# Optimization experiments

Hardware: AMD Instinct MI355X
Metric: run time of the kernel (lower is better)

Reference implementation:

```python
import jax, jax.numpy as jnp
import numpy as np

B, W, K = 16, 128, 128          # batch, window_size, n_features
KS = 7                          # conv kernel size
HG = 256                        # gru_hid_dim
HF = 256                        # forecast_hid_dim
HR = 256                        # recon_hid_dim
OUT = 128                       # out_dim
ALPHA = 0.2                     # leaky relu slope
ED = 2 * W                      # gatv2 embed dims (2*window == 2*features here == 256)


def setup_inputs() -> dict:
    key = jax.random.key(0)
    ks = jax.random.split(key, 32)
    s = lambda k, shp, sc=0.05: (jax.random.normal(k, shp, dtype=jnp.float32) * sc)
    return {
        "x": jax.random.normal(ks[0], (B, W, K), dtype=jnp.float32),
        # ConvLayer
        "conv_w": s(ks[1], (K, K, KS)),
        "conv_b": s(ks[2], (K,)),
        # FeatureAttentionLayer (gatv2): lin 2W->2W, a (2W,1), bias (K,K)
        "fg_lin_w": s(ks[3], (ED, 2 * W)),
        "fg_lin_b": s(ks[4], (ED,)),
        "fg_a": s(ks[5], (ED, 1)),
        "fg_bias": s(ks[6], (K, K)),
        # TemporalAttentionLayer (gatv2): lin 2K->2K, a (2K,1), bias (W,W)
        "tg_lin_w": s(ks[7], (2 * K, 2 * K)),
        "tg_lin_b": s(ks[8], (2 * K,)),
        "tg_a": s(ks[9], (2 * K, 1)),
        "tg_bias": s(ks[10], (W, W)),
        # GRU encoder: input 3K -> HG (torch gate order r,z,n)
        "gru_w_ih": s(ks[11], (3 * HG, 3 * K)),
        "gru_w_hh": s(ks[12], (3 * HG, HG)),
        "gru_b_ih": s(ks[13], (3 * HG,)),
        "gru_b_hh": s(ks[14], (3 * HG,)),
        # Forecasting_Model (n_layers=1 -> two Linears)
        "fc1_w": s(ks[15], (HF, HG)),
        "fc1_b": s(ks[16], (HF,)),
        "fc2_w": s(ks[17], (OUT, HF)),
        "fc2_b": s(ks[18], (OUT,)),
        # ReconstructionModel: decoder GRU HG -> HR, fc HR -> OUT
        "dec_w_ih": s(ks[19], (3 * HR, HG)),
        "dec_w_hh": s(ks[20], (3 * HR, HR)),
        "dec_b_ih": s(ks[21], (3 * HR,)),
        "dec_b_hh": s(ks[22], (3 * HR,)),
        "rec_fc_w": s(ks[23], (OUT, HR)),
        "rec_fc_b": s(ks[24], (OUT,)),
    }


def _gru(x_seq, w_ih, w_hh, b_ih, b_hh):
    """torch-convention GRU over (b, t, d). Returns (outs (b,t,H), h_T (b,H))."""
    H = w_hh.shape[1]
    def step(h, xt):
        gi = xt @ w_ih.T + b_ih
        gh = h @ w_hh.T + b_hh
        ir, iz, inn = jnp.split(gi, 3, axis=-1)
        hr, hz, hn = jnp.split(gh, 3, axis=-1)
        r = jax.nn.sigmoid(ir + hr)
        z = jax.nn.sigmoid(iz + hz)
        n = jnp.tanh(inn + r * hn)
        h_new = (1.0 - z) * n + z * h
        return h_new, h_new
    h0 = jnp.zeros((x_seq.shape[0], H), x_seq.dtype)
    hT, outs = jax.lax.scan(step, h0, jnp.swapaxes(x_seq, 0, 1))
    return jnp.swapaxes(outs, 0, 1), hT


def _gatv2(v, lin_w, lin_b, a, bias):
    """v: (b, N, D). Pairwise concat GATv2 attention, returns sigmoid(attn @ v)."""
    b, N, D = v.shape
    vi = jnp.broadcast_to(v[:, :, None, :], (b, N, N, D))   # node i repeated
    vj = jnp.broadcast_to(v[:, None, :, :], (b, N, N, D))   # node j alternating
    cat = jnp.concatenate([vi, vj], axis=-1)                 # (b, N, N, 2D)
    h = jax.nn.leaky_relu(cat @ lin_w.T + lin_b, ALPHA)      # (b, N, N, ED)
    e = jnp.squeeze(h @ a, -1) + bias                        # (b, N, N)
    attn = jax.nn.softmax(e, axis=2)
    return jax.nn.sigmoid(jnp.einsum('bij,bjd->bid', attn, v))


def reference(x, conv_w, conv_b, fg_lin_w, fg_lin_b, fg_a, fg_bias,
              tg_lin_w, tg_lin_b, tg_a, tg_bias,
              gru_w_ih, gru_w_hh, gru_b_ih, gru_b_hh,
              fc1_w, fc1_b, fc2_w, fc2_b,
              dec_w_ih, dec_w_hh, dec_b_ih, dec_b_hh, rec_fc_w, rec_fc_b):
    # ConvLayer: permute -> pad -> conv1d -> relu -> permute
    xc = jnp.transpose(x, (0, 2, 1))                        # (b, K, W)
    xc = jnp.pad(xc, ((0, 0), (0, 0), ((KS - 1) // 2, (KS - 1) // 2)))
    y = jax.lax.conv_general_dilated(xc, conv_w, (1,), 'VALID',
                                     dimension_numbers=('NCH', 'OIH', 'NCH'))
    xconv = jnp.transpose(jax.nn.relu(y + conv_b[None, :, None]), (0, 2, 1))  # (b, W, K)

    # Feature GAT operates on (b, K, W); output permuted back to (b, W, K)
    h_feat = jnp.transpose(
        _gatv2(jnp.transpose(xconv, (0, 2, 1)), fg_lin_w, fg_lin_b, fg_a, fg_bias),
        (0, 2, 1))
    # Temporal GAT operates on (b, W, K)
    h_temp = _gatv2(xconv, tg_lin_w, tg_lin_b, tg_a, tg_bias)

    h_cat = jnp.concatenate([xconv, h_feat, h_temp], axis=2)  # (b, W, 3K)
    _, h_end = _gru(h_cat, gru_w_ih, gru_w_hh, gru_b_ih, gru_b_hh)  # (b, HG)

    # Forecasting MLP (dropout is identity in eval)
    pred = jax.nn.relu(h_end @ fc1_w.T + fc1_b) @ fc2_w.T + fc2_b   # (b, OUT)

    # ReconstructionModel: repeat_interleave along dim=1 then view (b, W, HG)
    h_rep = jnp.repeat(h_end, W, axis=1).reshape(h_end.shape[0], W, -1)
    dec_out, _ = _gru(h_rep, dec_w_ih, dec_w_hh, dec_b_ih, dec_b_hh)  # (b, W, HR)
    recons = dec_out @ rec_fc_w.T + rec_fc_b                          # (b, W, OUT)

    return pred, recons
```

## Files before the change

### kernel.cpp

```cpp
#include <hip/hip_runtime.h>

typedef _Float16 f16;
typedef _Float16 f16x2 __attribute__((ext_vector_type(2)));
typedef _Float16 f16x4 __attribute__((ext_vector_type(4)));
typedef _Float16 f16x8 __attribute__((ext_vector_type(8)));
typedef float f32x4 __attribute__((ext_vector_type(4)));
typedef unsigned int ui4 __attribute__((ext_vector_type(4)));

__device__ __forceinline__ float fast_rcp(float x) {
#if __has_builtin(__builtin_amdgcn_rcpf)
    return __builtin_amdgcn_rcpf(x);
#else
    return 1.0f / x;
#endif
}
__device__ __forceinline__ float sigmoidf(float x) { return fast_rcp(1.0f + __expf(-x)); }
__device__ __forceinline__ float tanh_f(float x)   { return 2.0f * fast_rcp(1.0f + __expf(-2.0f * x)) - 1.0f; }

__device__ __forceinline__ unsigned int pk2(float a, float b) {
    union { _Float16 h[2]; unsigned int u; } t;
    t.h[0] = (_Float16)a; t.h[1] = (_Float16)b;
    return t.u;
}
__device__ __forceinline__ unsigned short f16bits(float f) {
    union { _Float16 h; unsigned short u; } t; t.h = (_Float16)f; return t.u;
}
__device__ __forceinline__ float dot2f(unsigned int wa, unsigned int hb, float c) {
#if __has_builtin(__builtin_amdgcn_fdot2)
    return __builtin_amdgcn_fdot2(__builtin_bit_cast(f16x2, wa),
                                  __builtin_bit_cast(f16x2, hb), c, false);
#else
    f16x2 a = __builtin_bit_cast(f16x2, wa), b = __builtin_bit_cast(f16x2, hb);
    return c + (float)a.x * (float)b.x + (float)a.y * (float)b.y;
#endif
}


__global__ void prep_kernel(const float* __restrict__ conv_w,
                            const float* __restrict__ fg_lin_w,
                            const float* __restrict__ tg_lin_w,
                            const float* __restrict__ w_ih,
                            const float* __restrict__ w_hh,
                            const float* __restrict__ dec_w_ih,
                            const float* __restrict__ dec_w_hh,
                            const float* __restrict__ rec_fc_w,
                            f16* __restrict__ w_ihB,
                            unsigned int* __restrict__ wpkE,
                            unsigned int* __restrict__ wpkD,
                            float* __restrict__ c01,
                            float* __restrict__ linTf, float* __restrict__ linTt,
                            float* __restrict__ recT, float* __restrict__ convT)
{
    const int blk = blockIdx.x, lane = threadIdx.x;
    const int quad = lane >> 4, lq = lane & 15;
    if (blk < 576) {
        int tau = blk / 12, kk = blk % 12;
        int g = tau % 3, jt = tau / 3;
        int n = g * 256 + jt * 16 + lq;
        int k0 = kk * 32 + quad * 8;
        f16x8 v;
#pragma unroll
        for (int e = 0; e < 8; ++e) v[e] = (f16)w_ih[n * 384 + k0 + e];
        *(f16x8*)&w_ihB[(blk * 64 + lane) * 8] = v;
    } else if (blk < 960) {
        int i2 = blk - 576;
        const float* src = w_hh; unsigned int* dst = wpkE;
        if (i2 >= 192) { i2 -= 192; src = dec_w_hh; dst = wpkD; }
        int g = i2 >> 6, i = i2 & 63;
#pragma unroll
        for (int c = 0; c < 8; ++c) {
            int tidx = lane * 8 + c;
            int j = tidx >> 1, half = tidx & 1;
            int n = g * 256 + j, k = half * 128 + i * 2;
            dst[(g * 64 + i) * 512 + tidx] = pk2(src[n * 256 + k], src[n * 256 + k + 1]);
        }
    } else if (blk < 972) {
        int n = (blk - 960) * 64 + lane;
        float s0 = 0.f, s1 = 0.f;
        const float* row = dec_w_ih + (long)n * 256;
        for (int d = 0; d < 128; ++d) { s0 += row[d]; s1 += row[128 + d]; }
        c01[n] = s0; c01[768 + n] = s1;
    } else if (blk < 1484) {
        int i = blk - 972; int mat = i >> 8, d = i & 255;
        const float* src = mat ? tg_lin_w : fg_lin_w;
        float* dst = mat ? linTt : linTf;
#pragma unroll
        for (int c = 0; c < 4; ++c) { int n = lane + 64 * c; dst[d * 256 + n] = src[n * 256 + d]; }
    } else if (blk < 1740) {
        int d = blk - 1484;
#pragma unroll
        for (int c = 0; c < 2; ++c) { int j2 = lane + 64 * c; recT[d * 128 + j2] = rec_fc_w[j2 * 256 + d]; }
    } else {
        int i = blk - 1740;
#pragma unroll
        for (int c = 0; c < 2; ++c) { int co = lane + 64 * c; convT[i * 128 + co] = conv_w[co * 896 + i]; }
    }
}

__global__ void conv_kernel(const float* __restrict__ x,
                            const float* __restrict__ convT,
                            const float* __restrict__ cb,
                            float* __restrict__ h_catT,
                            float* __restrict__ xconvT)
{
    const int wc = blockIdx.x, b = blockIdx.y, tid = threadIdx.x;
    __shared__ float xs[14][128];
    const int w0 = wc * 8;
#pragma unroll
    for (int i = 0; i < 14; ++i) {
        int row = w0 - 3 + i;
        xs[i][tid] = (row >= 0 && row < 128) ? x[(b * 128 + row) * 128 + tid] : 0.f;
    }
    __syncthreads();
    float bias = cb[tid];
    float acc[8];
#pragma unroll
    for (int j = 0; j < 8; ++j) acc[j] = bias;
    for (int ci = 0; ci < 128; ++ci) {
        float wv[7];
#pragma unroll
        for (int t = 0; t < 7; ++t) wv[t] = convT[(ci * 7 + t) * 128 + tid];
#pragma unroll
        for (int t = 0; t < 7; ++t) {
#pragma unroll
            for (int j = 0; j < 8; ++j) acc[j] += xs[j + t][ci] * wv[t];
        }
    }
#pragma unroll
    for (int j = 0; j < 8; ++j) {
        float v = fmaxf(acc[j], 0.f);
        h_catT[((w0 + j) * 16 + b) * 384 + tid] = v;
        xconvT[(b * 128 + tid) * 128 + w0 + j] = v;
    }
}

__global__ void lin_kernel(const float* __restrict__ vsrc, int mode,
                           const float* __restrict__ T,
                           const float* __restrict__ lb,
                           float* __restrict__ P, float* __restrict__ Q)
{
    const int tid = threadIdx.x;
    const int row0 = blockIdx.x * 8;
    __shared__ __align__(16) float vs[8][128];
    if (mode == 0) {
        ((float4*)vs)[tid] = ((const float4*)(vsrc + row0 * 128))[tid];
    } else {
        int b = row0 >> 7;
        int rr = tid >> 5, q = tid & 31;
        int t = (row0 & 127) + rr;
        *(float4*)&vs[rr][q * 4] = *(const float4*)&vsrc[(t * 16 + b) * 384 + q * 4];
    }
    __syncthreads();
    const int n = tid;
    float bias = lb[n];
    float accP[8], accQ[8];
#pragma unroll
    for (int rr = 0; rr < 8; ++rr) { accP[rr] = bias; accQ[rr] = 0.f; }
    for (int d4 = 0; d4 < 32; ++d4) {
        float4 vv[8];
#pragma unroll
        for (int rr = 0; rr < 8; ++rr) vv[rr] = *(const float4*)&vs[rr][d4 * 4];
#pragma unroll
        for (int e = 0; e < 4; ++e) {
            float wP = T[(d4 * 4 + e) * 256 + n];
            float wQ = T[(128 + d4 * 4 + e) * 256 + n];
#pragma unroll
            for (int rr = 0; rr < 8; ++rr) {
                float h = (e == 0) ? vv[rr].x : (e == 1) ? vv[rr].y : (e == 2) ? vv[rr].z : vv[rr].w;
                accP[rr] += h * wP;
                accQ[rr] += h * wQ;
            }
        }
    }
#pragma unroll
    for (int rr = 0; rr < 8; ++rr) {
        P[(long)(row0 + rr) * 256 + n] = accP[rr];
        Q[(long)(row0 + rr) * 256 + n] = accQ[rr];
    }
}

__global__ void gat_kernel(const float* __restrict__ P, const float* __restrict__ Q,
                           const float* __restrict__ a,
                           const float* __restrict__ bias,
                           const float* __restrict__ vbase,
                           float* __restrict__ h_catT, int mode)
{
    const int bid = blockIdx.x;
    const int b = bid >> 7, i = bid & 127;
    const int tid = threadIdx.x;
    __shared__ __align__(16) float Ps[256], as_[256], ej[128], red[8], op[256];
    __shared__ __align__(16) float buf[16384];

    Ps[tid]  = P[(long)(b * 128 + i) * 256 + tid];
    as_[tid] = a[tid];

    const int jl = tid >> 3, c = tid & 7;
    for (int j0 = 0; j0 < 128; j0 += 32) {
        __syncthreads();
#pragma unroll
        for (int r = 0; r < 8; ++r) {
            int flat = r * 256 + tid;
            int jj = flat >> 6, e4 = flat & 63;
            *(float4*)&buf[jj * 264 + e4 * 4] =
                *(const float4*)&Q[(long)(b * 128 + j0 + jj) * 256 + e4 * 4];
        }
        __syncthreads();
        float p = 0.f;
        for (int k = 0; k < 32; ++k) {
            int e = c + 8 * k;
            float hv = Ps[e] + buf[jl * 264 + e];
            hv = (hv > 0.f) ? hv : 0.2f * hv;
            p += hv * as_[e];
        }
        p += __shfl_xor(p, 1);
        p += __shfl_xor(p, 2);
        p += __shfl_xor(p, 4);
        if (c == 0) ej[j0 + jl] = p + bias[i * 128 + j0 + jl];
    }
    __syncthreads();
    {
        float v = (tid < 128) ? ej[tid] : -1e30f;
#pragma unroll
        for (int off = 32; off >= 1; off >>= 1) v = fmaxf(v, __shfl_xor(v, off));
        if ((tid & 63) == 0) red[tid >> 6] = v;
        __syncthreads();
        float m = fmaxf(fmaxf(red[0], red[1]), fmaxf(red[2], red[3]));
        float p = (tid < 128) ? __expf(ej[tid] - m) : 0.f;
        float s = p;
#pragma unroll
        for (int off = 32; off >= 1; off >>= 1) s += __shfl_xor(s, off);
        if ((tid & 63) == 0) red[4 + (tid >> 6)] = s;
        __syncthreads();
        float rs = fast_rcp(red[4] + red[5] + red[6] + red[7]);
        if (tid < 128) ej[tid] = p * rs;
        __syncthreads();
    }
    if (mode == 0) {
        const float4* s = (const float4*)(vbase + (long)b * 16384);
#pragma unroll
        for (int i2 = 0; i2 < 16; ++i2) ((float4*)buf)[i2 * 256 + tid] = s[i2 * 256 + tid];
    } else {
        int row = tid >> 1, hf = tid & 1;
#pragma unroll
        for (int i2 = 0; i2 < 16; ++i2) {
            int cc = (hf * 16 + i2) * 4;
            *(float4*)&buf[row * 128 + cc] = *(const float4*)&vbase[(row * 16 + b) * 384 + cc];
        }
    }
    __syncthreads();
    const int half = tid >> 7, d = tid & 127;
    float p0 = 0.f, p1 = 0.f, p2 = 0.f, p3 = 0.f;
#pragma unroll 4
    for (int j = 0; j < 64; j += 4) {
        int jb = half * 64 + j;
        p0 += ej[jb]     * buf[(jb)     * 128 + d];
        p1 += ej[jb + 1] * buf[(jb + 1) * 128 + d];
        p2 += ej[jb + 2] * buf[(jb + 2) * 128 + d];
        p3 += ej[jb + 3] * buf[(jb + 3) * 128 + d];
    }
    op[tid] = (p0 + p1) + (p2 + p3);
    __syncthreads();
    if (tid < 128) {
        float o = sigmoidf(op[tid] + op[tid + 128]);
        if (mode == 0)
            h_catT[(tid * 16 + b) * 384 + 128 + i] = o;
        else
            h_catT[(i * 16 + b) * 384 + 256 + tid] = o;
    }
}

__global__ void __launch_bounds__(256)
gi_gemm32(const float* __restrict__ h_catT, const f16* __restrict__ w_ihB,
          const float* __restrict__ b_ih, float* __restrict__ gi)
{
    const int t = blockIdx.x, tid = threadIdx.x;
    const int w = tid >> 6, lane = tid & 63, quad = lane >> 4, lq = lane & 15;
    __shared__ __align__(16) f16 hA[16][392];
    {
        int rr = tid >> 4, ii = tid & 15;
#pragma unroll
        for (int i2 = 0; i2 < 6; ++i2) {
            int cc = (ii * 6 + i2) * 4;
            float4 v = *(const float4*)&h_catT[(t * 16 + rr) * 384 + cc];
            f16x4 h; h[0] = (f16)v.x; h[1] = (f16)v.y; h[2] = (f16)v.z; h[3] = (f16)v.w;
            *(f16x4*)&hA[rr][cc] = h;
        }
    }
    int nidx[12];
    float biasv[12];
#pragma unroll
    for (int ti = 0; ti < 12; ++ti) {
        int tau = w * 12 + ti, g = tau % 3, jt = tau / 3;
        nidx[ti] = g * 256 + jt * 16 + lq;
        biasv[ti] = b_ih[nidx[ti]];
    }
    f32x4 acc[12] = {};
    __syncthreads();
    for (int kk = 0; kk < 12; ++kk) {
        f16x8 A = *(const f16x8*)&hA[lq][kk * 32 + quad * 8];
#pragma unroll
        for (int ti = 0; ti < 12; ++ti) {
            f16x8 B = *(const f16x8*)&w_ihB[(((w * 12 + ti) * 12 + kk) * 64 + lane) * 8];
            acc[ti] = __builtin_amdgcn_mfma_f32_16x16x32_f16(A, B, acc[ti], 0, 0, 0);
        }
    }
#pragma unroll
    for (int ti = 0; ti < 12; ++ti)
#pragma unroll
        for (int r = 0; r < 4; ++r) {
            int m = quad * 4 + r;
            gi[((long)m * 128 + t) * 768 + nidx[ti]] = acc[ti][r] + biasv[ti];
        }
}

__global__ void __launch_bounds__(512, 2)
gru16_kernel(const float* __restrict__ gi,
             const unsigned int* __restrict__ wpkE,
             const float* __restrict__ b_hh,
             const float* __restrict__ c01,
             const float* __restrict__ dec_b_ih,
             const unsigned int* __restrict__ wpkD,
             const float* __restrict__ dec_b_hh,
             float* __restrict__ h_end,
             float* __restrict__ dec_out)
{
    const int b    = blockIdx.x;
    const int tid  = threadIdx.x;
    const int j    = tid >> 1;
    const int half = tid & 1;

    __shared__ __align__(16) unsigned short hpk[2][256];
    __shared__ float he[256];
    __shared__ __align__(16) float gich[32 * 768];

    unsigned int wr[3][64];
    float bh[3];
#pragma unroll
    for (int g = 0; g < 3; ++g) {
        bh[g] = b_hh[g * 256 + j];
#pragma unroll
        for (int i = 0; i < 64; ++i) wr[g][i] = wpkE[(g * 64 + i) * 512 + tid];
    }
    if (tid < 256) { hpk[0][tid] = 0; hpk[1][tid] = 0; }
    float h = 0.f;

    const float* gib = gi + (long)b * 128 * 768;
    const unsigned int* hbase0 = ((const unsigned int*)hpk[0]) + half * 64;
    const unsigned int* hbase1 = ((const unsigned int*)hpk[1]) + half * 64;

    for (int cchunk = 0; cchunk < 4; ++cchunk) {
        const float* gsrc = gib + (long)cchunk * 32 * 768;
#pragma unroll
        for (int i = 0; i < 12; ++i) {
            int idx = (i * 512 + tid) * 4;
            *(float4*)&gich[idx] = *(const float4*)&gsrc[idx];
        }
        __syncthreads();
        for (int tt = 0; tt < 32; ++tt) {
            const int t = cchunk * 32 + tt;
            const int par = t & 1;
            float g0 = gich[tt * 768 + j];
            float g1 = gich[tt * 768 + 256 + j];
            float g2 = gich[tt * 768 + 512 + j];
            float aa0[4] = {}, aa1[4] = {}, aa2[4] = {};
            const ui4* hp = (const ui4*)(par ? hbase1 : hbase0);
#pragma unroll
            for (int i = 0; i < 16; ++i) {
                ui4 hv = hp[i];
#pragma unroll
                for (int e = 0; e < 4; ++e) {
                    aa0[e] = dot2f(wr[0][i * 4 + e], hv[e], aa0[e]);
                    aa1[e] = dot2f(wr[1][i * 4 + e], hv[e], aa1[e]);
                    aa2[e] = dot2f(wr[2][i * 4 + e], hv[e], aa2[e]);
                }
            }
            float a0 = (aa0[0] + aa0[1]) + (aa0[2] + aa0[3]);
            float a1 = (aa1[0] + aa1[1]) + (aa1[2] + aa1[3]);
            float a2 = (aa2[0] + aa2[1]) + (aa2[2] + aa2[3]);
            a0 += __shfl_xor(a0, 1);
            a1 += __shfl_xor(a1, 1);
            a2 += __shfl_xor(a2, 1);
            float rr = sigmoidf(g0 + a0 + bh[0]);
            float zz = sigmoidf(g1 + a1 + bh[1]);
            float nn = tanh_f  (g2 + rr * (a2 + bh[2]));
            h = (1.f - zz) * nn + zz * h;
            if (!half) hpk[par ^ 1][j] = f16bits(h);
            __syncthreads();
        }
    }

    if (!half) { he[j] = h; h_end[b * 256 + j] = h; }
    if (tid < 256) { hpk[0][tid] = 0; hpk[1][tid] = 0; }

    float c0[3], c1[3], bi[3];
#pragma unroll
    for (int g = 0; g < 3; ++g) {
        bh[g] = dec_b_hh[g * 256 + j];
        bi[g] = dec_b_ih[g * 256 + j];
        c0[g] = c01[g * 256 + j];
        c1[g] = c01[768 + g * 256 + j];
#pragma unroll
        for (int i = 0; i < 64; ++i) wr[g][i] = wpkD[(g * 64 + i) * 512 + tid];
    }
    h = 0.f;
    float* decbuf = gich;
    __syncthreads();

    for (int cchunk = 0; cchunk < 4; ++cchunk) {
        for (int tt = 0; tt < 32; ++tt) {
            const int t = cchunk * 32 + tt;
            const int par = t & 1;
            float e0 = he[2 * t], e1 = he[2 * t + 1];
            float aa0[4] = {}, aa1[4] = {}, aa2[4] = {};
            const ui4* hp = (const ui4*)(par ? hbase1 : hbase0);
#pragma unroll
            for (int i = 0; i < 16; ++i) {
                ui4 hv = hp[i];
#pragma unroll
                for (int e = 0; e < 4; ++e) {
                    aa0[e] = dot2f(wr[0][i * 4 + e], hv[e], aa0[e]);
                    aa1[e] = dot2f(wr[1][i * 4 + e], hv[e], aa1[e]);
                    aa2[e] = dot2f(wr[2][i * 4 + e], hv[e], aa2[e]);
                }
            }
            float a0 = (aa0[0] + aa0[1]) + (aa0[2] + aa0[3]);
            float a1 = (aa1[0] + aa1[1]) + (aa1[2] + aa1[3]);
            float a2 = (aa2[0] + aa2[1]) + (aa2[2] + aa2[3]);
            a0 += __shfl_xor(a0, 1);
            a1 += __shfl_xor(a1, 1);
            a2 += __shfl_xor(a2, 1);
            float rr = sigmoidf(e0 * c0[0] + e1 * c1[0] + bi[0] + a0 + bh[0]);
            float zz = sigmoidf(e0 * c0[1] + e1 * c1[1] + bi[1] + a1 + bh[1]);
            float nn = tanh_f  (e0 * c0[2] + e1 * c1[2] + bi[2] + rr * (a2 + bh[2]));
            h = (1.f - zz) * nn + zz * h;
            if (!half) {
                hpk[par ^ 1][j] = f16bits(h);
                decbuf[tt * 256 + j] = h;
            }
            __syncthreads();
        }
#pragma unroll
        for (int i = 0; i < 4; ++i) {
            int idx = (i * 512 + tid) * 4;
            *(float4*)&dec_out[(long)b * 32768 + cchunk * 8192 + idx] = *(const float4*)&decbuf[idx];
        }
        __syncthreads();
    }
}

__global__ void mlp_kernel(const float* __restrict__ h_end,
                           const float* __restrict__ fc1_w,
                           const float* __restrict__ fc1_b,
                           const float* __restrict__ fc2_w,
                           const float* __restrict__ fc2_b,
                           float* __restrict__ out)
{
    const int b = blockIdx.x, tid = threadIdx.x;
    __shared__ __align__(16) float hv[256], hid[256];
    hv[tid] = h_end[b * 256 + tid];
    __syncthreads();
    float acc = fc1_b[tid], acc2 = 0.f;
    const float4* wr = (const float4*)(fc1_w + tid * 256);
#pragma unroll 4
    for (int i = 0; i < 64; i += 2) {
        float4 w0 = wr[i], w1 = wr[i + 1];
        float4 h0 = *(const float4*)&hv[i * 4], h1 = *(const float4*)&hv[i * 4 + 4];
        acc  += w0.x * h0.x + w0.y * h0.y + w0.z * h0.z + w0.w * h0.w;
        acc2 += w1.x * h1.x + w1.y * h1.y + w1.z * h1.z + w1.w * h1.w;
    }
    hid[tid] = fmaxf(acc + acc2, 0.f);
    __syncthreads();
    if (tid < 128) {
        float a2 = fc2_b[tid], a3 = 0.f;
        const float4* w2 = (const float4*)(fc2_w + tid * 256);
#pragma unroll 4
        for (int i = 0; i < 64; i += 2) {
            float4 w0 = w2[i], w1 = w2[i + 1];
            float4 h0 = *(const float4*)&hid[i * 4], h1 = *(const float4*)&hid[i * 4 + 4];
            a2 += w0.x * h0.x + w0.y * h0.y + w0.z * h0.z + w0.w * h0.w;
            a3 += w1.x * h1.x + w1.y * h1.y + w1.z * h1.z + w1.w * h1.w;
        }
        out[b * 128 + tid] = a2 + a3;
    }
}

__global__ void recon_kernel(const float* __restrict__ dec_out,
                             const float* __restrict__ recT,
                             const float* __restrict__ rec_b,
                             float* __restrict__ out)
{
    const int blk = blockIdx.x, tid = threadIdx.x;
    __shared__ __align__(16) float dv[8][256];
#pragma unroll
    for (int i = 0; i < 2; ++i)
        ((float4*)dv)[i * 256 + tid] = ((const float4*)(dec_out + blk * 2048))[i * 256 + tid];
    __syncthreads();
    const int j = tid & 127, rh = tid >> 7;
    float acc[4];
#pragma unroll
    for (int rr = 0; rr < 4; ++rr) acc[rr] = rec_b[j];
    for (int d4 = 0; d4 < 64; ++d4) {
        float4 vv[4];
#pragma unroll
        for (int rr = 0; rr < 4; ++rr) vv[rr] = *(const float4*)&dv[rh * 4 + rr][d4 * 4];
#pragma unroll
        for (int e = 0; e < 4; ++e) {
            float wv = recT[(d4 * 4 + e) * 128 + j];
#pragma unroll
            for (int rr = 0; rr < 4; ++rr) {
                float h = (e == 0) ? vv[rr].x : (e == 1) ? vv[rr].y : (e == 2) ? vv[rr].z : vv[rr].w;
                acc[rr] += h * wv;
            }
        }
    }
#pragma unroll
    for (int rr = 0; rr < 4; ++rr)
        out[(blk * 8 + rh * 4 + rr) * 128 + j] = acc[rr];
}

extern "C" void kernel_launch(void* const* d_in, const int* in_sizes, int n_in,
                              void* d_out, int out_size, void* d_ws, size_t ws_size,
                              hipStream_t stream)
{
    const float* x        = (const float*)d_in[0];
    const float* conv_w   = (const float*)d_in[1];
    const float* conv_b   = (const float*)d_in[2];
    const float* fg_lin_w = (const float*)d_in[3];
    const float* fg_lin_b = (const float*)d_in[4];
    const float* fg_a     = (const float*)d_in[5];
    const float* fg_bias  = (const float*)d_in[6];
    const float* tg_lin_w = (const float*)d_in[7];
    const float* tg_lin_b = (const float*)d_in[8];
    const float* tg_a     = (const float*)d_in[9];
    const float* tg_bias  = (const float*)d_in[10];
    const float* gru_w_ih = (const float*)d_in[11];
    const float* gru_w_hh = (const float*)d_in[12];
    const float* gru_b_ih = (const float*)d_in[13];
    const float* gru_b_hh = (const float*)d_in[14];
    const float* fc1_w    = (const float*)d_in[15];
    const float* fc1_b    = (const float*)d_in[16];
    const float* fc2_w    = (const float*)d_in[17];
    const float* fc2_b    = (const float*)d_in[18];
    const float* dec_w_ih = (const float*)d_in[19];
    const float* dec_w_hh = (const float*)d_in[20];
    const float* dec_b_ih = (const float*)d_in[21];
    const float* dec_b_hh = (const float*)d_in[22];
    const float* rec_fc_w = (const float*)d_in[23];
    const float* rec_fc_b = (const float*)d_in[24];
    float* out = (float*)d_out;

    float* ws      = (float*)d_ws;
    float* h_catT  = ws;
    float* xconvT  = ws + 786432;
    float* Pf      = ws + 1048576;
    float* Qf      = ws + 1572864;
    float* Pt      = ws + 2097152;
    float* Qt      = ws + 2621440;
    float* gi      = Pf;
    f16*   w_ihB   = (f16*)(ws + 3932160);
    unsigned int* wpkE = (unsigned int*)(ws + 4079616);
    unsigned int* wpkD = (unsigned int*)(ws + 4177920);
    float* c01     = ws + 4276224;
    float* linTf   = ws + 4374528;
    float* linTt   = ws + 4440064;
    float* recT    = ws + 4505600;
    float* h_end   = ws + 4538368;
    float* dec_out = ws + 4542464;
    float* convT   = dec_out;

    prep_kernel<<<2636, 64, 0, stream>>>(conv_w, fg_lin_w, tg_lin_w, gru_w_ih, gru_w_hh,
                                         dec_w_ih, dec_w_hh, rec_fc_w,
                                         w_ihB, wpkE, wpkD, c01, linTf, linTt, recT, convT);
    conv_kernel<<<dim3(16, 16), 128, 0, stream>>>(x, convT, conv_b, h_catT, xconvT);
    lin_kernel<<<256, 256, 0, stream>>>(xconvT, 0, linTf, fg_lin_b, Pf, Qf);
    lin_kernel<<<256, 256, 0, stream>>>(h_catT, 1, linTt, tg_lin_b, Pt, Qt);
    gat_kernel<<<2048, 256, 0, stream>>>(Pf, Qf, fg_a, fg_bias, xconvT, h_catT, 0);
    gat_kernel<<<2048, 256, 0, stream>>>(Pt, Qt, tg_a, tg_bias, h_catT, h_catT, 1);
    gi_gemm32<<<128, 256, 0, stream>>>(h_catT, w_ihB, gru_b_ih, gi);
    gru16_kernel<<<16, 512, 0, stream>>>(gi, wpkE, gru_b_hh, c01, dec_b_ih, wpkD,
                                         dec_b_hh, h_end, dec_out);
    mlp_kernel<<<16, 256, 0, stream>>>(h_end, fc1_w, fc1_b, fc2_w, fc2_b, out);
    recon_kernel<<<256, 256, 0, stream>>>(dec_out, recT, rec_fc_b, out + 2048);
}
```

Before: 718.6 us.

## Split GRU into encoder/decoder kernels with 4-way K split and DPP reduce

Restructures the recurrent GRU so each thread covers two hidden units across six gate rows and a quarter of the K dimension, instead of one unit and half of K. The per-thread dot-product chains get shorter, the cross-lane reduction uses a DPP quad reduce, and the shared h buffer is padded to avoid bank conflicts. The fused encoder/decoder kernel is split into two launches, which frees shared memory in the decoder but adds a launch and a round trip of h_end through global memory. The register footprint stays at 192 weights per thread.

```diff
diff --git a/kernel.cpp b/kernel.cpp
--- a/kernel.cpp
+++ b/kernel.cpp
@@ -32,6 +32,19 @@
 #else
     f16x2 a = __builtin_bit_cast(f16x2, wa), b = __builtin_bit_cast(f16x2, hb);
     return c + (float)a.x * (float)b.x + (float)a.y * (float)b.y;
+#endif
+}
+__device__ __forceinline__ float quad_reduce(float x) {
+#if __has_builtin(__builtin_amdgcn_mov_dpp)
+    int a = __builtin_amdgcn_mov_dpp(__builtin_bit_cast(int, x), 0xB1, 0xF, 0xF, true);
+    x += __builtin_bit_cast(float, a);
+    int b = __builtin_amdgcn_mov_dpp(__builtin_bit_cast(int, x), 0x4E, 0xF, 0xF, true);
+    x += __builtin_bit_cast(float, b);
+    return x;
+#else
+    x += __shfl_xor(x, 1);
+    x += __shfl_xor(x, 2);
+    return x;
 #endif
 }
 
@@ -66,13 +79,14 @@
         int i2 = blk - 576;
         const float* src = w_hh; unsigned int* dst = wpkE;
         if (i2 >= 192) { i2 -= 192; src = dec_w_hh; dst = wpkD; }
-        int g = i2 >> 6, i = i2 & 63;
+        int r = i2 >> 5, i = i2 & 31;
 #pragma unroll
         for (int c = 0; c < 8; ++c) {
             int tidx = lane * 8 + c;
-            int j = tidx >> 1, half = tidx & 1;
-            int n = g * 256 + j, k = half * 128 + i * 2;
-            dst[(g * 64 + i) * 512 + tidx] = pk2(src[n * 256 + k], src[n * 256 + k + 1]);
+            int jt = tidx >> 2, q = tidx & 3;
+            int n = (r >> 1) * 256 + (r & 1) * 128 + jt;
+            int k = q * 64 + 2 * i;
+            dst[(r * 32 + i) * 512 + tidx] = pk2(src[n * 256 + k], src[n * 256 + k + 1]);
         }
     } else if (blk < 972) {
         int n = (blk - 960) * 64 + lane;
@@ -314,39 +328,29 @@
 }
 
 __global__ void __launch_bounds__(512, 2)
-gru16_kernel(const float* __restrict__ gi,
-             const unsigned int* __restrict__ wpkE,
-             const float* __restrict__ b_hh,
-             const float* __restrict__ c01,
-             const float* __restrict__ dec_b_ih,
-             const unsigned int* __restrict__ wpkD,
-             const float* __restrict__ dec_b_hh,
-             float* __restrict__ h_end,
-             float* __restrict__ dec_out)
-{
-    const int b    = blockIdx.x;
-    const int tid  = threadIdx.x;
-    const int j    = tid >> 1;
-    const int half = tid & 1;
-
-    __shared__ __align__(16) unsigned short hpk[2][256];
-    __shared__ float he[256];
+gru_enc(const float* __restrict__ gi,
+        const unsigned int* __restrict__ wpk,
+        const float* __restrict__ b_hh,
+        float* __restrict__ h_end)
+{
+    const int b = blockIdx.x, tid = threadIdx.x;
+    const int jt = tid >> 2, q = tid & 3;
+    __shared__ __align__(16) unsigned short hpk[2][296];
     __shared__ __align__(16) float gich[32 * 768];
 
-    unsigned int wr[3][64];
-    float bh[3];
-#pragma unroll
-    for (int g = 0; g < 3; ++g) {
-        bh[g] = b_hh[g * 256 + j];
-#pragma unroll
-        for (int i = 0; i < 64; ++i) wr[g][i] = wpkE[(g * 64 + i) * 512 + tid];
-    }
-    if (tid < 256) { hpk[0][tid] = 0; hpk[1][tid] = 0; }
-    float h = 0.f;
-
+    unsigned int wr[6][32];
+    float bh[6];
+    int nidx[6];
+#pragma unroll
+    for (int r = 0; r < 6; ++r) {
+        nidx[r] = (r >> 1) * 256 + (r & 1) * 128 + jt;
+        bh[r] = b_hh[nidx[r]];
+#pragma unroll
+        for (int i = 0; i < 32; ++i) wr[r][i] = wpk[(r * 32 + i) * 512 + tid];
+    }
+    for (int i = tid; i < 2 * 296; i += 512) ((unsigned short*)hpk)[i] = 0;
+    float h0 = 0.f, h1 = 0.f;
     const float* gib = gi + (long)b * 128 * 768;
-    const unsigned int* hbase0 = ((const unsigned int*)hpk[0]) + half * 64;
-    const unsigned int* hbase1 = ((const unsigned int*)hpk[1]) + half * 64;
 
     for (int cchunk = 0; cchunk < 4; ++cchunk) {
         const float* gsrc = gib + (long)cchunk * 32 * 768;
@@ -359,51 +363,75 @@
         for (int tt = 0; tt < 32; ++tt) {
             const int t = cchunk * 32 + tt;
             const int par = t & 1;
-            float g0 = gich[tt * 768 + j];
-            float g1 = gich[tt * 768 + 256 + j];
-            float g2 = gich[tt * 768 + 512 + j];
-            float aa0[4] = {}, aa1[4] = {}, aa2[4] = {};
-            const ui4* hp = (const ui4*)(par ? hbase1 : hbase0);
-#pragma unroll
-            for (int i = 0; i < 16; ++i) {
+            float gv[6];
+#pragma unroll
+            for (int r = 0; r < 6; ++r) gv[r] = gich[tt * 768 + nidx[r]];
+            float aa[6][2] = {};
+            const ui4* hp = (const ui4*)&hpk[par][q * 72];
+#pragma unroll
+            for (int i = 0; i < 8; ++i) {
                 ui4 hv = hp[i];
 #pragma unroll
                 for (int e = 0; e < 4; ++e) {
-                    aa0[e] = dot2f(wr[0][i * 4 + e], hv[e], aa0[e]);
-                    aa1[e] = dot2f(wr[1][i * 4 + e], hv[e], aa1[e]);
-                    aa2[e] = dot2f(wr[2][i * 4 + e], hv[e], aa2[e]);
+#pragma unroll
+                    for (int r = 0; r < 6; ++r)
+                        aa[r][e & 1] = dot2f(wr[r][i * 4 + e], hv[e], aa[r][e & 1]);
                 }
             }
-            float a0 = (aa0[0] + aa0[1]) + (aa0[2] + aa0[3]);
-            float a1 = (aa1[0] + aa1[1]) + (aa1[2] + aa1[3]);
-            float a2 = (aa2[0] + aa2[1]) + (aa2[2] + aa2[3]);
-            a0 += __shfl_xor(a0, 1);
-            a1 += __shfl_xor(a1, 1);
-            a2 += __shfl_xor(a2, 1);
-            float rr = sigmoidf(g0 + a0 + bh[0]);
-            float zz = sigmoidf(g1 + a1 + bh[1]);
-            float nn = tanh_f  (g2 + rr * (a2 + bh[2]));
-            h = (1.f - zz) * nn + zz * h;
-            if (!half) hpk[par ^ 1][j] = f16bits(h);
+            float s[6];
+#pragma unroll
+            for (int r = 0; r < 6; ++r) s[r] = quad_reduce(aa[r][0] + aa[r][1]);
+            float r0 = sigmoidf(gv[0] + s[0] + bh[0]);
+            float r1 = sigmoidf(gv[1] + s[1] + bh[1]);
+            float z0 = sigmoidf(gv[2] + s[2] + bh[2]);
+            float z1 = sigmoidf(gv[3] + s[3] + bh[3]);
+            float n0 = tanh_f(gv[4] + r0 * (s[4] + bh[4]));
+            float n1 = tanh_f(gv[5] + r1 * (s[5] + bh[5]));
+            h0 = (1.f - z0) * n0 + z0 * h0;
+            h1 = (1.f - z1) * n1 + z1 * h1;
+            if (q == 0) {
+                hpk[par ^ 1][(jt >> 6) * 72 + (jt & 63)]       = f16bits(h0);
+                hpk[par ^ 1][(2 + (jt >> 6)) * 72 + (jt & 63)] = f16bits(h1);
+            }
             __syncthreads();
         }
     }
-
-    if (!half) { he[j] = h; h_end[b * 256 + j] = h; }
-    if (tid < 256) { hpk[0][tid] = 0; hpk[1][tid] = 0; }
-
-    float c0[3], c1[3], bi[3];
-#pragma unroll
-    for (int g = 0; g < 3; ++g) {
-        bh[g] = dec_b_hh[g * 256 + j];
-        bi[g] = dec_b_ih[g * 256 + j];
-        c0[g] = c01[g * 256 + j];
-        c1[g] = c01[768 + g * 256 + j];
-#pragma unroll
-        for (int i = 0; i < 64; ++i) wr[g][i] = wpkD[(g * 64 + i) * 512 + tid];
-    }
-    h = 0.f;
-    float* decbuf = gich;
+    if (q == 0) {
+        h_end[b * 256 + jt]       = h0;
+        h_end[b * 256 + 128 + jt] = h1;
+    }
+}
+
+__global__ void __launch_bounds__(512, 2)
+gru_dec(const float* __restrict__ h_end,
+        const unsigned int* __restrict__ wpk,
+        const float* __restrict__ dec_b_hh,
+        const float* __restrict__ c01,
+        const float* __restrict__ dec_b_ih,
+        float* __restrict__ dec_out)
+{
+    const int b = blockIdx.x, tid = threadIdx.x;
+    const int jt = tid >> 2, q = tid & 3;
+    __shared__ __align__(16) unsigned short hpk[2][296];
+    __shared__ float he[256];
+    __shared__ __align__(16) float decbuf[32 * 256];
+
+    unsigned int wr[6][32];
+    float bh[6], c0[6], c1[6], bi[6];
+    int nidx[6];
+#pragma unroll
+    for (int r = 0; r < 6; ++r) {
+        nidx[r] = (r >> 1) * 256 + (r & 1) * 128 + jt;
+        bh[r] = dec_b_hh[nidx[r]];
+        bi[r] = dec_b_ih[nidx[r]];
+        c0[r] = c01[nidx[r]];
+        c1[r] = c01[768 + nidx[r]];
+#pragma unroll
+        for (int i = 0; i < 32; ++i) wr[r][i] = wpk[(r * 32 + i) * 512 + tid];
+    }
+    for (int i = tid; i < 2 * 296; i += 512) ((unsigned short*)hpk)[i] = 0;
+    if (tid < 256) he[tid] = h_end[b * 256 + tid];
+    float h0 = 0.f, h1 = 0.f;
     __syncthreads();
 
     for (int cchunk = 0; cchunk < 4; ++cchunk) {
@@ -411,31 +439,37 @@
             const int t = cchunk * 32 + tt;
             const int par = t & 1;
             float e0 = he[2 * t], e1 = he[2 * t + 1];
-            float aa0[4] = {}, aa1[4] = {}, aa2[4] = {};
-            const ui4* hp = (const ui4*)(par ? hbase1 : hbase0);
-#pragma unroll
-            for (int i = 0; i < 16; ++i) {
+            float aa[6][2] = {};
+            const ui4* hp = (const ui4*)&hpk[par][q * 72];
+#pragma unroll
+            for (int i = 0; i < 8; ++i) {
                 ui4 hv = hp[i];
 #pragma unroll
                 for (int e = 0; e < 4; ++e) {
-                    aa0[e] = dot2f(wr[0][i * 4 + e], hv[e], aa0[e]);
-                    aa1[e] = dot2f(wr[1][i * 4 + e], hv[e], aa1[e]);
-                    aa2[e] = dot2f(wr[2][i * 4 + e], hv[e], aa2[e]);
+#pragma unroll
+                    for (int r = 0; r < 6; ++r)
+                        aa[r][e & 1] = dot2f(wr[r][i * 4 + e], hv[e], aa[r][e & 1]);
                 }
             }
-            float a0 = (aa0[0] + aa0[1]) + (aa0[2] + aa0[3]);
-            float a1 = (aa1[0] + aa1[1]) + (aa1[2] + aa1[3]);
-            float a2 = (aa2[0] + aa2[1]) + (aa2[2] + aa2[3]);
-            a0 += __shfl_xor(a0, 1);
-            a1 += __shfl_xor(a1, 1);
-            a2 += __shfl_xor(a2, 1);
-            float rr = sigmoidf(e0 * c0[0] + e1 * c1[0] + bi[0] + a0 + bh[0]);
-            float zz = sigmoidf(e0 * c0[1] + e1 * c1[1] + bi[1] + a1 + bh[1]);
-            float nn = tanh_f  (e0 * c0[2] + e1 * c1[2] + bi[2] + rr * (a2 + bh[2]));
-            h = (1.f - zz) * nn + zz * h;
-            if (!half) {
-                hpk[par ^ 1][j] = f16bits(h);
-                decbuf[tt * 256 + j] = h;
+            float s[6], giv[6];
+#pragma unroll
+            for (int r = 0; r < 6; ++r) {
+                s[r] = quad_reduce(aa[r][0] + aa[r][1]);
+                giv[r] = e0 * c0[r] + e1 * c1[r] + bi[r];
+            }
+            float r0 = sigmoidf(giv[0] + s[0] + bh[0]);
+            float r1 = sigmoidf(giv[1] + s[1] + bh[1]);
+            float z0 = sigmoidf(giv[2] + s[2] + bh[2]);
+            float z1 = sigmoidf(giv[3] + s[3] + bh[3]);
+            float n0 = tanh_f(giv[4] + r0 * (s[4] + bh[4]));
+            float n1 = tanh_f(giv[5] + r1 * (s[5] + bh[5]));
+            h0 = (1.f - z0) * n0 + z0 * h0;
+            h1 = (1.f - z1) * n1 + z1 * h1;
+            if (q == 0) {
+                hpk[par ^ 1][(jt >> 6) * 72 + (jt & 63)]       = f16bits(h0);
+                hpk[par ^ 1][(2 + (jt >> 6)) * 72 + (jt & 63)] = f16bits(h1);
+                decbuf[tt * 256 + jt]       = h0;
+                decbuf[tt * 256 + 128 + jt] = h1;
             }
             __syncthreads();
         }
@@ -577,8 +611,8 @@
     gat_kernel<<<2048, 256, 0, stream>>>(Pf, Qf, fg_a, fg_bias, xconvT, h_catT, 0);
     gat_kernel<<<2048, 256, 0, stream>>>(Pt, Qt, tg_a, tg_bias, h_catT, h_catT, 1);
     gi_gemm32<<<128, 256, 0, stream>>>(h_catT, w_ihB, gru_b_ih, gi);
-    gru16_kernel<<<16, 512, 0, stream>>>(gi, wpkE, gru_b_hh, c01, dec_b_ih, wpkD,
-                                         dec_b_hh, h_end, dec_out);
+    gru_enc<<<16, 512, 0, stream>>>(gi, wpkE, gru_b_hh, h_end);
     mlp_kernel<<<16, 256, 0, stream>>>(h_end, fc1_w, fc1_b, fc2_w, fc2_b, out);
+    gru_dec<<<16, 512, 0, stream>>>(h_end, wpkD, dec_b_hh, c01, dec_b_ih, dec_out);
     recon_kernel<<<256, 256, 0, stream>>>(dec_out, recT, rec_fc_b, out + 2048);
 }
```

New measurement: 707.9 us. Within noise of the previous version (-1.5%).
